# Optimization experiments

Hardware: AMD Instinct MI355X
Metric: run time of the kernel (lower is better)

## Reference

```python
import jax, jax.numpy as jnp
import numpy as np
from jax import lax

B, C, H, W = 32, 3, 128, 128   # batch, image channels, event spatial dims
PC = 16                         # conditioning distribution_params channels
HID = 64                        # hidden channels of each parallel CNN
NUP = 2                         # number of upsampling stages
DN = ('NCHW', 'OIHW', 'NCHW')

BASE_SLICE = (slice(0, None, 2), slice(0, None, 2))
UP_SLICES = [(slice(1, None, 2), slice(1, None, 2)),
             (slice(0, None, 2), slice(1, None, 2)),
             (slice(1, None, 2), slice(0, None, 2))]


def setup_inputs() -> dict:
    key = jax.random.key(0)
    k0, k1, k2, k3 = jax.random.split(key, 4)
    n_nets = C + NUP * 3 * C  # 3 base + 18 upsampling nets = 21
    cin = C + PC
    return {
        'value': jax.random.uniform(k0, (B, C, H, W), jnp.float32),
        'distribution_params': jax.random.normal(k1, (B, PC, H, W), jnp.float32),
        'W1': jax.random.normal(k2, (n_nets, HID, cin, 3, 3), jnp.float32) * 0.05,
        'b1': jnp.zeros((n_nets, HID), jnp.float32),
        'W2': jax.random.normal(k3, (n_nets, 1, HID, 1, 1), jnp.float32) * 0.05,
        'b2': jnp.zeros((n_nets, 1), jnp.float32),
    }


def _cnn(x, w1, bb1, w2, bb2):
    # Conv3x3 -> ReLU -> Conv1x1, producing Bernoulli logits [B,1,h,w]
    h = lax.conv_general_dilated(x, w1, (1, 1), 'SAME', dimension_numbers=DN)
    h = jax.nn.relu(h + bb1[None, :, None, None])
    o = lax.conv_general_dilated(h, w2, (1, 1), 'SAME', dimension_numbers=DN)
    return o + bb2[None, :, None, None]


def _log_prob_block(imgs, params, masked, sl, idxs, W1, b1, W2, b2):
    lp = jnp.float32(0.0)
    for c, idx in enumerate(idxs):
        net_in = jnp.concatenate([masked, params], axis=1)
        logits = _cnn(net_in, W1[idx], b1[idx], W2[idx], b2[idx])[:, 0, sl[0], sl[1]]
        x = imgs[:, c, sl[0], sl[1]]
        # Bernoulli log-prob with logits, summed over batch and spatial dims
        lp = lp + jnp.sum(x * jax.nn.log_sigmoid(logits)
                          + (1.0 - x) * jax.nn.log_sigmoid(-logits))
        masked = masked.at[:, c, sl[0], sl[1]].set(x)
    return lp, masked


def reference(value, distribution_params, W1, b1, W2, b2):
    r = 2 ** NUP
    base = value[:, :, ::r, ::r]
    base_dp = distribution_params[:, :, ::r, ::r]
    masked = jnp.zeros_like(base)
    lp, masked = _log_prob_block(base, base_dp, masked, BASE_SLICE,
                                 list(range(C)), W1, b1, W2, b2)
    for level in range(NUP):
        rr = 2 ** (NUP - level - 1)
        v = value[:, :, ::rr, ::rr]
        dp = distribution_params[:, :, ::rr, ::rr]
        m = jnp.zeros_like(v)
        m = m.at[:, :, BASE_SLICE[0], BASE_SLICE[1]].set(
            v[:, :, BASE_SLICE[0], BASE_SLICE[1]])
        for s in range(3):
            idxs = [C + level * 3 * C + s * C + c for c in range(C)]
            blp, m = _log_prob_block(v, dp, m, UP_SLICES[s], idxs, W1, b1, W2, b2)
            lp = lp + blp
    return lp
```

## Files before the change

### kernel.cpp

```cpp
#include <hip/hip_runtime.h>

typedef unsigned char uchar;
typedef unsigned long long ull;
typedef __attribute__((ext_vector_type(2))) unsigned long long ullx2;
typedef __attribute__((ext_vector_type(4))) float floatx4;
typedef __attribute__((ext_vector_type(4))) unsigned int uintx4;

#define NB_IMG 18496
#define WHALF 9216
#define AREG 29408
#define NBLK 5856
#define NPART (NBLK * 8)

__device__ __forceinline__ uchar f2e4(float x) {
    float a = fabsf(x);
    unsigned s = (__float_as_uint(x) >> 24) & 0x80u;
    if (a >= 448.f) return (uchar)(s | 0x7E);
    if (a < 0.015625f) {
        int m = (int)rintf(a * 512.f);
        return (uchar)(s | (unsigned)m);
    }
    unsigned u = __float_as_uint(a);
    unsigned r = u + 0x7FFFFu + ((u >> 20) & 1u);
    unsigned e8 = (r >> 23) - 120u;
    return (uchar)(s | (e8 << 3) | ((r >> 20) & 7u));
}

__device__ __forceinline__ float row16sum(float v) {
    v += __int_as_float(__builtin_amdgcn_update_dpp(0, __float_as_int(v), 0x128, 0xf, 0xf, false));
    v += __int_as_float(__builtin_amdgcn_update_dpp(0, __float_as_int(v), 0x124, 0xf, 0xf, false));
    v += __int_as_float(__builtin_amdgcn_update_dpp(0, __float_as_int(v), 0x122, 0xf, 0xf, false));
    v += __int_as_float(__builtin_amdgcn_update_dpp(0, __float_as_int(v), 0x121, 0xf, 0xf, false));
    return v;
}

__device__ __forceinline__ void eval_geom(int e, int& sy0, int& sx0, int& cch, int& s_idx) {
    if (e < 3) { sy0 = 0; sx0 = 0; cch = e; s_idx = -1; }
    else {
        int u = e - 3; int s = (u % 9) / 3; cch = u % 3; s_idx = s;
        sy0 = (s == 1) ? 0 : 1;
        sx0 = (s == 2) ? 0 : 1;
    }
}

__device__ __forceinline__ bool tap_active(int e, int ci, int dy, int dx,
                                           int sy0, int sx0, int cch, int s_idx) {
    if (ci >= 3) return true;
    int py = (sy0 + dy - 1) & 1;
    int px = (sx0 + dx - 1) & 1;
    if (e < 3) return (py == 0 && px == 0) && (ci < cch);
    if (py == 0 && px == 0) return true;
    int sp = (py == 1 && px == 1) ? 0 : ((py == 0 && px == 1) ? 1 : 2);
    return (sp < s_idx) || (sp == s_idx && ci < cch);
}

__global__ __launch_bounds__(256) void prep_kernel(
    const float* __restrict__ value, const float* __restrict__ dp,
    const float* __restrict__ W1,
    uchar* __restrict__ imgbf, uchar* __restrict__ wbfA, uchar* __restrict__ wbfB)
{
    const int bid = blockIdx.x;
    if (bid < 578) {
        const int t = bid * 256 + threadIdx.x;
        const int b = t / 4624;
        const int r = t - b * 4624;
        const int y = r / 34;
        const int xh4 = r - y * 34;
        const int yi = y - 4;
        uchar* dst = imgbf + ((size_t)b * NB_IMG + (size_t)y * 136) * 32;

        if ((unsigned)yi < 128u && xh4 >= 1 && xh4 <= 32) {
            const int xi0 = 4 * xh4 - 4;
            const float* vb = value + (size_t)b * 3 * 16384 + yi * 128 + xi0;
            const float* pb = dp + (size_t)b * 16 * 16384 + yi * 128 + xi0;
            floatx4 ch[19];
            #pragma unroll
            for (int i = 0; i < 3; ++i)  ch[i]     = *(const floatx4*)(vb + i * 16384);
            #pragma unroll
            for (int i = 0; i < 16; ++i) ch[3 + i] = *(const floatx4*)(pb + i * 16384);
            #pragma unroll
            for (int e = 0; e < 4; ++e) {
                unsigned d[8];
                #pragma unroll
                for (int i = 0; i < 8; ++i) d[i] = 0;
                #pragma unroll
                for (int ci = 0; ci < 19; ++ci)
                    d[ci >> 2] |= (unsigned)f2e4(ch[ci][e]) << ((ci & 3) * 8);
                uchar* ds = dst + (((e & 1) * 68) + 2 * xh4 + (e >> 1)) * 32;
                uintx4 v0, v1;
                v0[0] = d[0]; v0[1] = d[1]; v0[2] = d[2]; v0[3] = d[3];
                v1[0] = d[4]; v1[1] = d[5]; v1[2] = d[6]; v1[3] = d[7];
                *(uintx4*)ds = v0;
                *(uintx4*)(ds + 16) = v1;
            }
        } else {
            uintx4 z; z[0] = 0; z[1] = 0; z[2] = 0; z[3] = 0;
            #pragma unroll
            for (int e = 0; e < 4; ++e) {
                uchar* ds = dst + (((e & 1) * 68) + 2 * xh4 + (e >> 1)) * 32;
                *(uintx4*)ds = z;
                *(uintx4*)(ds + 16) = z;
            }
        }
    } else {
        const int q = bid - 578;
        const int e = q / 9, tap = q % 9;
        const int g = threadIdx.x >> 6, n = threadIdx.x & 63;
        int sy0, sx0, cch, s_idx;
        eval_geom(e, sy0, sx0, cch, s_idx);
        const int dy = tap / 3, dx = tap % 3;
        const float* wrow = W1 + ((size_t)e * 64 + n) * 171;
        ull v = 0;
        #pragma unroll
        for (int qq = 0; qq < 8; ++qq) {
            const int ci = g * 8 + qq;
            float w = 0.f;
            if (ci < 19 && tap_active(e, ci, dy, dx, sy0, sx0, cch, s_idx))
                w = wrow[ci * 9 + tap];
            v |= (ull)f2e4(w) << (qq * 8);
        }
        if (n < 32) *(ull*)&wbfA[(size_t)e * WHALF + ((tap * 4 + g) * 32 + n) * 8] = v;
        else        *(ull*)&wbfB[(size_t)e * WHALF + ((tap * 4 + g) * 32 + (n - 32)) * 8] = v;
    }
}

struct SW { ullx2 a, b; };

__device__ __forceinline__ void sw_load(int tid, SW& r, const uchar* wbfB, int e) {
    const uchar* src = wbfB + (size_t)e * WHALF;
    r.a = *(const ullx2*)(src + tid * 16);
    if (tid < 64) r.b = *(const ullx2*)(src + (512 + tid) * 16);
}
__device__ __forceinline__ void sw_write(int tid, uchar* dst, const SW& r) {
    *(ullx2*)(dst + tid * 16) = r.a;
    if (tid < 64) *(ullx2*)(dst + (512 + tid) * 16) = r.b;
}

template<int SY0, int SX0, int RSH, int OWSH, int TXH, int TY>
__device__ __forceinline__ void run_eval(
    int e, int c, int b, int oy0, int ox0, int tid, int bid,
    uchar* Alds, uchar* Wb,
    const uchar* __restrict__ imgbf, const uchar* __restrict__ wbfA,
    const uchar* __restrict__ wbfB, const float* __restrict__ value,
    const float* __restrict__ b1, const float* __restrict__ W2,
    const float* __restrict__ b2, float* __restrict__ partials)
{
    constexpr int TPIX = TY * 2 * TXH;
    constexpr int OW = 1 << OWSH;
    const int lane = tid & 63, w = tid >> 6;
    const int l15 = lane & 15, l4 = lane >> 4;
    const int wfb = l4 * 256 + l15 * 8;

    SW sw;
    sw_load(tid, sw, wbfB, e);

    const int yb = 2 * oy0 - 1, xb = 2 * ox0 - 2;
    const uchar* img_b = imgbf + (size_t)b * ((size_t)NB_IMG * 32);
    #pragma unroll
    for (int i = 0; i < (TPIX + 511) / 512; ++i) {
        const int px = tid + i * 512;
        if (px < TPIX) {
            const int typ = px / TXH;
            const int xh = px - typ * TXH;
            const int yl = yb + (typ >> 1);
            const int xl = xb + 2 * xh + (typ & 1);
            int yi = (yl << RSH) + 4; yi = yi < 0 ? 0 : (yi > 135 ? 135 : yi);
            int xi = (xl << RSH) + 4; xi = xi < 0 ? 0 : (xi > 135 ? 135 : xi);
            const uchar* src = img_b + (size_t)(yi * 136 + (xi & 1) * 68 + (xi >> 1)) * 32;
            ullx2 v01 = *(const ullx2*)src;
            ull v2 = *(const ull*)(src + 16);
            uchar* dst = Alds + px * 24;
            *(ull*)dst = v01[0];
            *(ull*)(dst + 8) = v01[1];
            *(ull*)(dst + 16) = v2;
        }
    }
    if (tid < 4) *(ull*)(Alds + TPIX * 24 + tid * 8) = 0ull;
    sw_write(tid, Wb, sw);
    __syncthreads();

    const uchar* wA = wbfA + (size_t)e * WHALF;
    ull breg[9][2];
    #pragma unroll
    for (int tap = 0; tap < 9; ++tap) {
        breg[tap][0] = *(const ull*)(wA + tap * 1024 + wfb);
        breg[tap][1] = *(const ull*)(wA + tap * 1024 + wfb + 128);
    }
    float b1c[4], w2c[4];
    #pragma unroll
    for (int nb = 0; nb < 4; ++nb) {
        b1c[nb] = b1[e * 64 + nb * 16 + l15];
        w2c[nb] = W2[e * 64 + nb * 16 + l15];
    }
    const float bias2 = b2[e];

    int abase[2];
    #pragma unroll
    for (int a = 0; a < 2; ++a) {
        const int row = w * 32 + a * 16 + l15;
        const int oy = row >> OWSH, ox = row & (OW - 1);
        abase[a] = ((SY0 + 2 * oy) * 2 * TXH + ox) * 24 + l4 * 8;
    }

    floatx4 acc[2][4];
    #pragma unroll
    for (int a = 0; a < 2; ++a)
        #pragma unroll
        for (int nb = 0; nb < 4; ++nb)
            acc[a][nb] = (floatx4){0.f, 0.f, 0.f, 0.f};

    __builtin_amdgcn_s_setprio(1);
    #pragma unroll
    for (int tap = 0; tap < 9; ++tap) {
        const int dy = tap / 3, dx = tap % 3;
        const int v = SX0 + dx + 1;
        const int D = (2 * dy + (v & 1)) * TXH + (v >> 1);
        ull av[2];
        #pragma unroll
        for (int a = 0; a < 2; ++a)
            av[a] = *(const ull*)(Alds + abase[a] + D * 24);
        const ull bv2 = *(const ull*)(Wb + wfb + tap * 1024);
        const ull bv3 = *(const ull*)(Wb + wfb + tap * 1024 + 128);
        #pragma unroll
        for (int a = 0; a < 2; ++a) {
            acc[a][0] = __builtin_amdgcn_mfma_f32_16x16x32_fp8_fp8((long)av[a], (long)breg[tap][0], acc[a][0], 0, 0, 0);
            acc[a][1] = __builtin_amdgcn_mfma_f32_16x16x32_fp8_fp8((long)av[a], (long)breg[tap][1], acc[a][1], 0, 0, 0);
            acc[a][2] = __builtin_amdgcn_mfma_f32_16x16x32_fp8_fp8((long)av[a], (long)bv2, acc[a][2], 0, 0, 0);
            acc[a][3] = __builtin_amdgcn_mfma_f32_16x16x32_fp8_fp8((long)av[a], (long)bv3, acc[a][3], 0, 0, 0);
        }
    }
    __builtin_amdgcn_s_setprio(0);

    float zv[8];
    #pragma unroll
    for (int a = 0; a < 2; ++a)
        #pragma unroll
        for (int j = 0; j < 4; ++j) {
            float part = 0.f;
            #pragma unroll
            for (int nb = 0; nb < 4; ++nb)
                part += w2c[nb] * fmaxf(acc[a][nb][j] + b1c[nb], 0.f);
            zv[a * 4 + j] = row16sum(part);
        }
    float lpsum = 0.f;
    if (l15 < 8) {
        const float u0 = (l15 & 1) ? zv[1] : zv[0];
        const float u1 = (l15 & 1) ? zv[3] : zv[2];
        const float u2 = (l15 & 1) ? zv[5] : zv[4];
        const float u3 = (l15 & 1) ? zv[7] : zv[6];
        const float p0 = (l15 & 2) ? u1 : u0;
        const float p1 = (l15 & 2) ? u3 : u2;
        const float zs = ((l15 & 4) ? p1 : p0) + bias2;
        const int row = w * 32 + ((l15 >> 2) << 4) + (l4 << 2) + (l15 & 3);
        const int oyj = oy0 + (row >> OWSH);
        const int oxj = ox0 + (row & (OW - 1));
        const int yj = (SY0 + 2 * oyj) << RSH;
        const int xj = (SX0 + 2 * oxj) << RSH;
        const float xv = value[((size_t)b * 3 + c) * 16384 + yj * 128 + xj];
        const float az = fabsf(zs);
        const float t2 = __builtin_amdgcn_exp2f(-1.442695041f * az);
        const float l1p = 0.69314718056f * __builtin_amdgcn_logf(1.f + t2);
        lpsum = xv * zs + fminf(-zs, 0.f) - l1p;
    }

    lpsum += __shfl_down(lpsum, 32);
    lpsum += __shfl_down(lpsum, 16);
    lpsum += __shfl_down(lpsum, 8);
    lpsum += __shfl_down(lpsum, 4);
    lpsum += __shfl_down(lpsum, 2);
    lpsum += __shfl_down(lpsum, 1);
    if (lane == 0) partials[bid * 8 + w] = lpsum;
}

__global__ __launch_bounds__(512) void pcnn_all(
    const uchar* __restrict__ imgbf, const uchar* __restrict__ wbfA,
    const uchar* __restrict__ wbfB, const float* __restrict__ value,
    const float* __restrict__ b1, const float* __restrict__ W2,
    const float* __restrict__ b2, float* __restrict__ partials)
{
    __shared__ __align__(16) uchar smem[AREG + WHALF];
    uchar* Alds = smem;
    uchar* Wb   = smem + AREG;
    const int bid = blockIdx.x, tid = threadIdx.x;

    const int x = bid & 7, r = bid >> 3;
    const int g = r / 183, u = r - g * 183;
    const int b = g * 8 + x;

    if (u < 144) {
        const int sc = u >> 4, t = u & 15;
        const int s = sc / 3, c = sc - 3 * s;
        const int e = 12 + sc;
        const int oy0 = (t >> 1) * 8, ox0 = (t & 1) * 32;
        if (s == 0)
            run_eval<1, 1, 0, 5, 34, 18>(e, c, b, oy0, ox0, tid, bid, Alds, Wb, imgbf, wbfA, wbfB, value, b1, W2, b2, partials);
        else if (s == 1)
            run_eval<0, 1, 0, 5, 34, 18>(e, c, b, oy0, ox0, tid, bid, Alds, Wb, imgbf, wbfA, wbfB, value, b1, W2, b2, partials);
        else
            run_eval<1, 0, 0, 5, 34, 18>(e, c, b, oy0, ox0, tid, bid, Alds, Wb, imgbf, wbfA, wbfB, value, b1, W2, b2, partials);
    } else if (u < 180) {
        const int v = u - 144;
        const int sc = v >> 2, t = v & 3;
        const int s = sc / 3, c = sc - 3 * s;
        const int e = 3 + sc;
        const int oy0 = t * 8;
        if (s == 0)
            run_eval<1, 1, 1, 5, 34, 18>(e, c, b, oy0, 0, tid, bid, Alds, Wb, imgbf, wbfA, wbfB, value, b1, W2, b2, partials);
        else if (s == 1)
            run_eval<0, 1, 1, 5, 34, 18>(e, c, b, oy0, 0, tid, bid, Alds, Wb, imgbf, wbfA, wbfB, value, b1, W2, b2, partials);
        else
            run_eval<1, 0, 1, 5, 34, 18>(e, c, b, oy0, 0, tid, bid, Alds, Wb, imgbf, wbfA, wbfB, value, b1, W2, b2, partials);
    } else {
        const int c = u - 180;
        run_eval<0, 0, 2, 4, 17, 33>(c, c, b, 0, 0, tid, bid, Alds, Wb, imgbf, wbfA, wbfB, value, b1, W2, b2, partials);
    }
}

__global__ __launch_bounds__(1024) void reduce_kernel(
    const floatx4* __restrict__ p4, float* __restrict__ out)
{
    __shared__ float ws[16];
    const int tid = threadIdx.x;
    float s = 0.f;
    for (int i = tid; i < NPART / 4; i += 1024) {
        floatx4 v = p4[i];
        s += v[0] + v[1] + v[2] + v[3];
    }
    s += __shfl_down(s, 32);
    s += __shfl_down(s, 16);
    s += __shfl_down(s, 8);
    s += __shfl_down(s, 4);
    s += __shfl_down(s, 2);
    s += __shfl_down(s, 1);
    if ((tid & 63) == 0) ws[tid >> 6] = s;
    __syncthreads();
    if (tid == 0) {
        float t = 0.f;
        #pragma unroll
        for (int i = 0; i < 16; ++i) t += ws[i];
        out[0] = t;
    }
}

extern "C" void kernel_launch(void* const* d_in, const int* in_sizes, int n_in,
                              void* d_out, int out_size, void* d_ws, size_t ws_size,
                              hipStream_t stream) {
    const float* value = (const float*)d_in[0];
    const float* dp    = (const float*)d_in[1];
    const float* W1    = (const float*)d_in[2];
    const float* b1    = (const float*)d_in[3];
    const float* W2    = (const float*)d_in[4];
    const float* b2    = (const float*)d_in[5];
    float* out = (float*)d_out;

    uchar* imgbf = (uchar*)d_ws;
    uchar* wbfA  = imgbf + (size_t)32 * NB_IMG * 32;
    uchar* wbfB  = wbfA + (size_t)21 * WHALF;
    float* partials = (float*)(wbfB + (size_t)21 * WHALF);

    hipLaunchKernelGGL(prep_kernel, dim3(767), dim3(256), 0, stream,
                       value, dp, W1, imgbf, wbfA, wbfB);
    hipLaunchKernelGGL(pcnn_all, dim3(NBLK), dim3(512), 0, stream,
                       imgbf, wbfA, wbfB, value, b1, W2, b2, partials);
    hipLaunchKernelGGL(reduce_kernel, dim3(1), dim3(1024), 0, stream,
                       (const floatx4*)partials, out);
}
```

Measured before the change: 85.11 us.

## Evaluate all three channel nets per block to reuse staged input tile

Each block now stages one image tile in LDS and runs the three per-channel networks of a slice against it, instead of one network per block. This removes the repeated input-tile staging across channels. Blocks shrink to 256 threads covering half the rows, and all three nets' B-half weights are staged in LDS. The trade-off is a larger LDS footprint per block (about 44 KB), which may lower occupancy, plus more work per block and a serial loop over channels.

```diff
diff --git a/kernel.cpp b/kernel.cpp
--- a/kernel.cpp
+++ b/kernel.cpp
@@ -8,9 +8,9 @@
 
 #define NB_IMG 18496
 #define WHALF 9216
-#define AREG 29408
-#define NBLK 5856
-#define NPART (NBLK * 8)
+#define AREG 16352
+#define NBLK 3904
+#define NPART4 3904
 
 __device__ __forceinline__ uchar f2e4(float x) {
     float a = fabsf(x);
@@ -124,22 +124,10 @@
     }
 }
 
-struct SW { ullx2 a, b; };
-
-__device__ __forceinline__ void sw_load(int tid, SW& r, const uchar* wbfB, int e) {
-    const uchar* src = wbfB + (size_t)e * WHALF;
-    r.a = *(const ullx2*)(src + tid * 16);
-    if (tid < 64) r.b = *(const ullx2*)(src + (512 + tid) * 16);
-}
-__device__ __forceinline__ void sw_write(int tid, uchar* dst, const SW& r) {
-    *(ullx2*)(dst + tid * 16) = r.a;
-    if (tid < 64) *(ullx2*)(dst + (512 + tid) * 16) = r.b;
-}
-
 template<int SY0, int SX0, int RSH, int OWSH, int TXH, int TY>
-__device__ __forceinline__ void run_eval(
-    int e, int c, int b, int oy0, int ox0, int tid, int bid,
-    uchar* Alds, uchar* Wb,
+__device__ __forceinline__ void run_class(
+    int e0, int b, int oy0, int ox0, int tid, int bid,
+    uchar* Alds, uchar* Wlds,
     const uchar* __restrict__ imgbf, const uchar* __restrict__ wbfA,
     const uchar* __restrict__ wbfB, const float* __restrict__ value,
     const float* __restrict__ b1, const float* __restrict__ W2,
@@ -151,14 +139,19 @@
     const int l15 = lane & 15, l4 = lane >> 4;
     const int wfb = l4 * 256 + l15 * 8;
 
-    SW sw;
-    sw_load(tid, sw, wbfB, e);
+    ullx2 swv[7];
+    const uchar* wsrc = wbfB + (size_t)e0 * WHALF;
+    #pragma unroll
+    for (int i = 0; i < 7; ++i) {
+        const int cc = tid + i * 256;
+        if (cc < 1728) swv[i] = *(const ullx2*)(wsrc + (size_t)cc * 16);
+    }
 
     const int yb = 2 * oy0 - 1, xb = 2 * ox0 - 2;
     const uchar* img_b = imgbf + (size_t)b * ((size_t)NB_IMG * 32);
     #pragma unroll
-    for (int i = 0; i < (TPIX + 511) / 512; ++i) {
-        const int px = tid + i * 512;
+    for (int i = 0; i < (TPIX + 255) / 256; ++i) {
+        const int px = tid + i * 256;
         if (px < TPIX) {
             const int typ = px / TXH;
             const int xh = px - typ * TXH;
@@ -176,23 +169,12 @@
         }
     }
     if (tid < 4) *(ull*)(Alds + TPIX * 24 + tid * 8) = 0ull;
-    sw_write(tid, Wb, sw);
+    #pragma unroll
+    for (int i = 0; i < 7; ++i) {
+        const int cc = tid + i * 256;
+        if (cc < 1728) *(ullx2*)(Wlds + (size_t)cc * 16) = swv[i];
+    }
     __syncthreads();
-
-    const uchar* wA = wbfA + (size_t)e * WHALF;
-    ull breg[9][2];
-    #pragma unroll
-    for (int tap = 0; tap < 9; ++tap) {
-        breg[tap][0] = *(const ull*)(wA + tap * 1024 + wfb);
-        breg[tap][1] = *(const ull*)(wA + tap * 1024 + wfb + 128);
-    }
-    float b1c[4], w2c[4];
-    #pragma unroll
-    for (int nb = 0; nb < 4; ++nb) {
-        b1c[nb] = b1[e * 64 + nb * 16 + l15];
-        w2c[nb] = W2[e * 64 + nb * 16 + l15];
-    }
-    const float bias2 = b2[e];
 
     int abase[2];
     #pragma unroll
@@ -202,65 +184,87 @@
         abase[a] = ((SY0 + 2 * oy) * 2 * TXH + ox) * 24 + l4 * 8;
     }
 
-    floatx4 acc[2][4];
-    #pragma unroll
-    for (int a = 0; a < 2; ++a)
-        #pragma unroll
-        for (int nb = 0; nb < 4; ++nb)
-            acc[a][nb] = (floatx4){0.f, 0.f, 0.f, 0.f};
-
-    __builtin_amdgcn_s_setprio(1);
-    #pragma unroll
-    for (int tap = 0; tap < 9; ++tap) {
-        const int dy = tap / 3, dx = tap % 3;
-        const int v = SX0 + dx + 1;
-        const int D = (2 * dy + (v & 1)) * TXH + (v >> 1);
-        ull av[2];
+    float lpsum = 0.f;
+
+    #pragma unroll
+    for (int c = 0; c < 3; ++c) {
+        const int e = e0 + c;
+        const uchar* wA = wbfA + (size_t)e * WHALF;
+        const uchar* Wb = Wlds + (size_t)c * WHALF;
+
+        ull breg[9][2];
+        #pragma unroll
+        for (int tap = 0; tap < 9; ++tap) {
+            breg[tap][0] = *(const ull*)(wA + tap * 1024 + wfb);
+            breg[tap][1] = *(const ull*)(wA + tap * 1024 + wfb + 128);
+        }
+        float b1c[4], w2c[4];
+        #pragma unroll
+        for (int nb = 0; nb < 4; ++nb) {
+            b1c[nb] = b1[e * 64 + nb * 16 + l15];
+            w2c[nb] = W2[e * 64 + nb * 16 + l15];
+        }
+        const float bias2 = b2[e];
+
+        floatx4 acc[2][4];
         #pragma unroll
         for (int a = 0; a < 2; ++a)
-            av[a] = *(const ull*)(Alds + abase[a] + D * 24);
-        const ull bv2 = *(const ull*)(Wb + wfb + tap * 1024);
-        const ull bv3 = *(const ull*)(Wb + wfb + tap * 1024 + 128);
-        #pragma unroll
-        for (int a = 0; a < 2; ++a) {
-            acc[a][0] = __builtin_amdgcn_mfma_f32_16x16x32_fp8_fp8((long)av[a], (long)breg[tap][0], acc[a][0], 0, 0, 0);
-            acc[a][1] = __builtin_amdgcn_mfma_f32_16x16x32_fp8_fp8((long)av[a], (long)breg[tap][1], acc[a][1], 0, 0, 0);
-            acc[a][2] = __builtin_amdgcn_mfma_f32_16x16x32_fp8_fp8((long)av[a], (long)bv2, acc[a][2], 0, 0, 0);
-            acc[a][3] = __builtin_amdgcn_mfma_f32_16x16x32_fp8_fp8((long)av[a], (long)bv3, acc[a][3], 0, 0, 0);
-        }
-    }
-    __builtin_amdgcn_s_setprio(0);
-
-    float zv[8];
-    #pragma unroll
-    for (int a = 0; a < 2; ++a)
-        #pragma unroll
-        for (int j = 0; j < 4; ++j) {
-            float part = 0.f;
             #pragma unroll
             for (int nb = 0; nb < 4; ++nb)
-                part += w2c[nb] * fmaxf(acc[a][nb][j] + b1c[nb], 0.f);
-            zv[a * 4 + j] = row16sum(part);
-        }
-    float lpsum = 0.f;
-    if (l15 < 8) {
-        const float u0 = (l15 & 1) ? zv[1] : zv[0];
-        const float u1 = (l15 & 1) ? zv[3] : zv[2];
-        const float u2 = (l15 & 1) ? zv[5] : zv[4];
-        const float u3 = (l15 & 1) ? zv[7] : zv[6];
-        const float p0 = (l15 & 2) ? u1 : u0;
-        const float p1 = (l15 & 2) ? u3 : u2;
-        const float zs = ((l15 & 4) ? p1 : p0) + bias2;
-        const int row = w * 32 + ((l15 >> 2) << 4) + (l4 << 2) + (l15 & 3);
-        const int oyj = oy0 + (row >> OWSH);
-        const int oxj = ox0 + (row & (OW - 1));
-        const int yj = (SY0 + 2 * oyj) << RSH;
-        const int xj = (SX0 + 2 * oxj) << RSH;
-        const float xv = value[((size_t)b * 3 + c) * 16384 + yj * 128 + xj];
-        const float az = fabsf(zs);
-        const float t2 = __builtin_amdgcn_exp2f(-1.442695041f * az);
-        const float l1p = 0.69314718056f * __builtin_amdgcn_logf(1.f + t2);
-        lpsum = xv * zs + fminf(-zs, 0.f) - l1p;
+                acc[a][nb] = (floatx4){0.f, 0.f, 0.f, 0.f};
+
+        __builtin_amdgcn_s_setprio(1);
+        #pragma unroll
+        for (int tap = 0; tap < 9; ++tap) {
+            const int dy = tap / 3, dx = tap % 3;
+            const int v = SX0 + dx + 1;
+            const int D = (2 * dy + (v & 1)) * TXH + (v >> 1);
+            ull av[2];
+            #pragma unroll
+            for (int a = 0; a < 2; ++a)
+                av[a] = *(const ull*)(Alds + abase[a] + D * 24);
+            const ull bv2 = *(const ull*)(Wb + wfb + tap * 1024);
+            const ull bv3 = *(const ull*)(Wb + wfb + tap * 1024 + 128);
+            #pragma unroll
+            for (int a = 0; a < 2; ++a) {
+                acc[a][0] = __builtin_amdgcn_mfma_f32_16x16x32_fp8_fp8((long)av[a], (long)breg[tap][0], acc[a][0], 0, 0, 0);
+                acc[a][1] = __builtin_amdgcn_mfma_f32_16x16x32_fp8_fp8((long)av[a], (long)breg[tap][1], acc[a][1], 0, 0, 0);
+                acc[a][2] = __builtin_amdgcn_mfma_f32_16x16x32_fp8_fp8((long)av[a], (long)bv2, acc[a][2], 0, 0, 0);
+                acc[a][3] = __builtin_amdgcn_mfma_f32_16x16x32_fp8_fp8((long)av[a], (long)bv3, acc[a][3], 0, 0, 0);
+            }
+        }
+        __builtin_amdgcn_s_setprio(0);
+
+        float zv[8];
+        #pragma unroll
+        for (int a = 0; a < 2; ++a)
+            #pragma unroll
+            for (int j = 0; j < 4; ++j) {
+                float part = 0.f;
+                #pragma unroll
+                for (int nb = 0; nb < 4; ++nb)
+                    part += w2c[nb] * fmaxf(acc[a][nb][j] + b1c[nb], 0.f);
+                zv[a * 4 + j] = row16sum(part);
+            }
+        if (l15 < 8) {
+            const float u0 = (l15 & 1) ? zv[1] : zv[0];
+            const float u1 = (l15 & 1) ? zv[3] : zv[2];
+            const float u2 = (l15 & 1) ? zv[5] : zv[4];
+            const float u3 = (l15 & 1) ? zv[7] : zv[6];
+            const float p0 = (l15 & 2) ? u1 : u0;
+            const float p1 = (l15 & 2) ? u3 : u2;
+            const float zs = ((l15 & 4) ? p1 : p0) + bias2;
+            const int row = w * 32 + ((l15 >> 2) << 4) + (l4 << 2) + (l15 & 3);
+            const int oyj = oy0 + (row >> OWSH);
+            const int oxj = ox0 + (row & (OW - 1));
+            const int yj = (SY0 + 2 * oyj) << RSH;
+            const int xj = (SX0 + 2 * oxj) << RSH;
+            const float xv = value[((size_t)b * 3 + c) * 16384 + yj * 128 + xj];
+            const float az = fabsf(zs);
+            const float t2 = __builtin_amdgcn_exp2f(-1.442695041f * az);
+            const float l1p = 0.69314718056f * __builtin_amdgcn_logf(1.f + t2);
+            lpsum += xv * zs + fminf(-zs, 0.f) - l1p;
+        }
     }
 
     lpsum += __shfl_down(lpsum, 32);
@@ -269,60 +273,58 @@
     lpsum += __shfl_down(lpsum, 4);
     lpsum += __shfl_down(lpsum, 2);
     lpsum += __shfl_down(lpsum, 1);
-    if (lane == 0) partials[bid * 8 + w] = lpsum;
-}
-
-__global__ __launch_bounds__(512) void pcnn_all(
+    if (lane == 0) partials[bid * 4 + w] = lpsum;
+}
+
+__global__ __launch_bounds__(256) void pcnn_all(
     const uchar* __restrict__ imgbf, const uchar* __restrict__ wbfA,
     const uchar* __restrict__ wbfB, const float* __restrict__ value,
     const float* __restrict__ b1, const float* __restrict__ W2,
     const float* __restrict__ b2, float* __restrict__ partials)
 {
-    __shared__ __align__(16) uchar smem[AREG + WHALF];
+    __shared__ __align__(16) uchar smem[AREG + 3 * WHALF];
     uchar* Alds = smem;
-    uchar* Wb   = smem + AREG;
+    uchar* Wlds = smem + AREG;
     const int bid = blockIdx.x, tid = threadIdx.x;
 
     const int x = bid & 7, r = bid >> 3;
-    const int g = r / 183, u = r - g * 183;
+    const int g = r / 122, u = r - g * 122;
     const int b = g * 8 + x;
 
-    if (u < 144) {
-        const int sc = u >> 4, t = u & 15;
-        const int s = sc / 3, c = sc - 3 * s;
-        const int e = 12 + sc;
-        const int oy0 = (t >> 1) * 8, ox0 = (t & 1) * 32;
+    if (u < 96) {
+        const int s = u >> 5, t = u & 31;
+        const int e0 = 12 + s * 3;
+        const int oy0 = (t >> 1) * 4, ox0 = (t & 1) * 32;
         if (s == 0)
-            run_eval<1, 1, 0, 5, 34, 18>(e, c, b, oy0, ox0, tid, bid, Alds, Wb, imgbf, wbfA, wbfB, value, b1, W2, b2, partials);
+            run_class<1, 1, 0, 5, 34, 10>(e0, b, oy0, ox0, tid, bid, Alds, Wlds, imgbf, wbfA, wbfB, value, b1, W2, b2, partials);
         else if (s == 1)
-            run_eval<0, 1, 0, 5, 34, 18>(e, c, b, oy0, ox0, tid, bid, Alds, Wb, imgbf, wbfA, wbfB, value, b1, W2, b2, partials);
+            run_class<0, 1, 0, 5, 34, 10>(e0, b, oy0, ox0, tid, bid, Alds, Wlds, imgbf, wbfA, wbfB, value, b1, W2, b2, partials);
         else
-            run_eval<1, 0, 0, 5, 34, 18>(e, c, b, oy0, ox0, tid, bid, Alds, Wb, imgbf, wbfA, wbfB, value, b1, W2, b2, partials);
-    } else if (u < 180) {
-        const int v = u - 144;
-        const int sc = v >> 2, t = v & 3;
-        const int s = sc / 3, c = sc - 3 * s;
-        const int e = 3 + sc;
-        const int oy0 = t * 8;
+            run_class<1, 0, 0, 5, 34, 10>(e0, b, oy0, ox0, tid, bid, Alds, Wlds, imgbf, wbfA, wbfB, value, b1, W2, b2, partials);
+    } else if (u < 120) {
+        const int v = u - 96;
+        const int s = v >> 3, t = v & 7;
+        const int e0 = 3 + s * 3;
+        const int oy0 = t * 4;
         if (s == 0)
-            run_eval<1, 1, 1, 5, 34, 18>(e, c, b, oy0, 0, tid, bid, Alds, Wb, imgbf, wbfA, wbfB, value, b1, W2, b2, partials);
+            run_class<1, 1, 1, 5, 34, 10>(e0, b, oy0, 0, tid, bid, Alds, Wlds, imgbf, wbfA, wbfB, value, b1, W2, b2, partials);
         else if (s == 1)
-            run_eval<0, 1, 1, 5, 34, 18>(e, c, b, oy0, 0, tid, bid, Alds, Wb, imgbf, wbfA, wbfB, value, b1, W2, b2, partials);
+            run_class<0, 1, 1, 5, 34, 10>(e0, b, oy0, 0, tid, bid, Alds, Wlds, imgbf, wbfA, wbfB, value, b1, W2, b2, partials);
         else
-            run_eval<1, 0, 1, 5, 34, 18>(e, c, b, oy0, 0, tid, bid, Alds, Wb, imgbf, wbfA, wbfB, value, b1, W2, b2, partials);
+            run_class<1, 0, 1, 5, 34, 10>(e0, b, oy0, 0, tid, bid, Alds, Wlds, imgbf, wbfA, wbfB, value, b1, W2, b2, partials);
     } else {
-        const int c = u - 180;
-        run_eval<0, 0, 2, 4, 17, 33>(c, c, b, 0, 0, tid, bid, Alds, Wb, imgbf, wbfA, wbfB, value, b1, W2, b2, partials);
-    }
-}
-
-__global__ __launch_bounds__(1024) void reduce_kernel(
+        const int t = u - 120;
+        run_class<0, 0, 2, 4, 18, 18>(0, b, t * 8, 0, tid, bid, Alds, Wlds, imgbf, wbfA, wbfB, value, b1, W2, b2, partials);
+    }
+}
+
+__global__ __launch_bounds__(256) void reduce_kernel(
     const floatx4* __restrict__ p4, float* __restrict__ out)
 {
-    __shared__ float ws[16];
+    __shared__ float ws[4];
     const int tid = threadIdx.x;
     float s = 0.f;
-    for (int i = tid; i < NPART / 4; i += 1024) {
+    for (int i = tid; i < NPART4; i += 256) {
         floatx4 v = p4[i];
         s += v[0] + v[1] + v[2] + v[3];
     }
@@ -334,12 +336,7 @@
     s += __shfl_down(s, 1);
     if ((tid & 63) == 0) ws[tid >> 6] = s;
     __syncthreads();
-    if (tid == 0) {
-        float t = 0.f;
-        #pragma unroll
-        for (int i = 0; i < 16; ++i) t += ws[i];
-        out[0] = t;
-    }
+    if (tid == 0) out[0] = ws[0] + ws[1] + ws[2] + ws[3];
 }
 
 extern "C" void kernel_launch(void* const* d_in, const int* in_sizes, int n_in,
@@ -360,8 +357,8 @@
 
     hipLaunchKernelGGL(prep_kernel, dim3(767), dim3(256), 0, stream,
                        value, dp, W1, imgbf, wbfA, wbfB);
-    hipLaunchKernelGGL(pcnn_all, dim3(NBLK), dim3(512), 0, stream,
+    hipLaunchKernelGGL(pcnn_all, dim3(NBLK), dim3(256), 0, stream,
                        imgbf, wbfA, wbfB, value, b1, W2, b2, partials);
-    hipLaunchKernelGGL(reduce_kernel, dim3(1), dim3(1024), 0, stream,
+    hipLaunchKernelGGL(reduce_kernel, dim3(1), dim3(256), 0, stream,
                        (const floatx4*)partials, out);
 }
```

After: 77.95 us. 1.09x faster.
